# Kernel tuning notes

Hardware: AMD Instinct MI355X
Metric: run time of the kernel (lower is better)

## Reference

```python
import jax, jax.numpy as jnp
import numpy as np

B, C, H, W = 16, 64, 128, 128
HX, HY = 64, 64


def _rnn_scan(x, Wih, Whh, bih, bhh):
    """Vanilla tanh RNN, batch_first. x: [N, T, Cin] -> [N, T, Hh]."""
    # precompute input projection with one big GEMM
    pre = jnp.einsum('ntc,hc->nth', x, Wih) + bih + bhh  # [N,T,Hh]
    N = x.shape[0]
    h0 = jnp.zeros((N, Whh.shape[0]), dtype=x.dtype)

    def step(h, p):
        h = jnp.tanh(p + h @ Whh.T)
        return h, h

    _, ys = jax.lax.scan(step, h0, jnp.swapaxes(pre, 0, 1))  # [T,N,Hh]
    return jnp.swapaxes(ys, 0, 1)


def setup_inputs() -> dict:
    key = jax.random.key(0)
    ks = jax.random.split(key, 9)
    sx = 1.0 / np.sqrt(HX)
    sy = 1.0 / np.sqrt(HY)
    return {
        'x': jax.random.normal(ks[0], (B, C, H, W), dtype=jnp.float32),
        'Wih_x': jax.random.uniform(ks[1], (HX, C), jnp.float32, -sx, sx),
        'Whh_x': jax.random.uniform(ks[2], (HX, HX), jnp.float32, -sx, sx),
        'bih_x': jax.random.uniform(ks[3], (HX,), jnp.float32, -sx, sx),
        'bhh_x': jax.random.uniform(ks[4], (HX,), jnp.float32, -sx, sx),
        'Wih_y': jax.random.uniform(ks[5], (HY, HX), jnp.float32, -sy, sy),
        'Whh_y': jax.random.uniform(ks[6], (HY, HY), jnp.float32, -sy, sy),
        'bih_y': jax.random.uniform(ks[7], (HY,), jnp.float32, -sy, sy),
        'bhh_y': jax.random.uniform(ks[8], (HY,), jnp.float32, -sy, sy),
    }


def reference(x, Wih_x, Whh_x, bih_x, bhh_x, Wih_y, Whh_y, bih_y, bhh_y):
    b, c, h, w = x.shape
    # X-axis RNN: scan along width, sequences are rows
    xw = jnp.transpose(x, (0, 2, 3, 1)).reshape(b * h, w, c)  # [B*H, W, C]
    out_x = _rnn_scan(xw, Wih_x, Whh_x, bih_x, bhh_x)          # [B*H, W, HX]
    # Y-axis RNN: scan along height, sequences are columns
    xy = out_x.reshape(b, h, w, HX)
    xy = jnp.transpose(xy, (0, 2, 1, 3)).reshape(b * w, h, HX)  # [B*W, H, HX]
    out_y = _rnn_scan(xy, Wih_y, Whh_y, bih_y, bhh_y)           # [B*W, H, HY]
    out = out_y.reshape(b, w, h, HY)
    return jnp.transpose(out, (0, 3, 2, 1))  # [B, HY, H, W]
```

## Files before the change

### kernel.cpp

```cpp
#include <hip/hip_runtime.h>
#include <stdint.h>


#define TLEN 128
#define NSEQ 2048
#define PSH (NSEQ*64)
#define GT 16

typedef __bf16   bf16x8 __attribute__((ext_vector_type(8)));
typedef _Float16 f16x8  __attribute__((ext_vector_type(8)));
typedef _Float16 f16x4  __attribute__((ext_vector_type(4)));
typedef float    f32x4  __attribute__((ext_vector_type(4)));
typedef unsigned short u16x4 __attribute__((ext_vector_type(4)));
typedef unsigned short u16x8 __attribute__((ext_vector_type(8)));

static __device__ __forceinline__ unsigned int fbits(float f){
    union { float f; unsigned int u; } v; v.f = f; return v.u;
}
static __device__ __forceinline__ float ubits(unsigned int u){
    union { unsigned int u; float f; } v; v.u = u; return v.f;
}
static __device__ __forceinline__ float bf2f(unsigned short s){ return ubits(((unsigned int)s) << 16); }
static __device__ __forceinline__ unsigned short f2bf(float f){
    unsigned int u = fbits(f);
    return (unsigned short)((u + 0x7FFFu + ((u >> 16) & 1u)) >> 16);
}
static __device__ __forceinline__ __bf16 us2b(unsigned short s){
    union { unsigned short u; __bf16 b; } v; v.u = s; return v.b;
}
static __device__ __forceinline__ unsigned short h2us(_Float16 h){
    union { _Float16 h; unsigned short s; } v; v.h = h; return v.s;
}
struct bfpair { __bf16 hi, lo; };
static __device__ __forceinline__ bfpair splitf(float f){
    unsigned short h = f2bf(f);
    bfpair r; r.hi = us2b(h); r.lo = us2b(f2bf(f - bf2f(h))); return r;
}
static __device__ __forceinline__ float fast_tanh(float x){
    float e = __builtin_amdgcn_exp2f(x * 2.8853900817779268f);
    return 1.0f - 2.0f * __builtin_amdgcn_rcpf(e + 1.0f);
}

__global__ __launch_bounds__(256) void k_proj0(const float* __restrict__ A,
                                               const float* __restrict__ Wih,
                                               const float* __restrict__ b1,
                                               const float* __restrict__ b2,
                                               _Float16* __restrict__ pre){
    __shared__ alignas(16) unsigned short lds_t[2][4][16][64];
    int lane = threadIdx.x & 63;
    int wv   = threadIdx.x >> 6;
    int q    = lane >> 4, l15 = lane & 15;

    bf16x8 Whi[4][2], Wlo[4][2];
#pragma unroll
    for (int n = 0; n < 4; n++)
#pragma unroll
        for (int kc = 0; kc < 2; kc++){
            const float* p = Wih + (n * 16 + l15) * 64 + kc * 32 + q * 8;
#pragma unroll
            for (int i = 0; i < 8; i++){
                bfpair s = splitf(p[i]);
                Whi[n][kc][i] = s.hi; Wlo[n][kc][i] = s.lo;
            }
        }
    float bias[4];
#pragma unroll
    for (int n = 0; n < 4; n++){
        int j = n * 16 + l15;
        bias[n] = b1[j] + b2[j];
    }

    int row0 = blockIdx.x * 128 + wv * 32;

    float av[2][2][8];
#pragma unroll
    for (int mi = 0; mi < 2; mi++){
        int r = row0 + mi * 16 + l15;
        int b = r >> 14, hw = r & 16383;
        const float* xb = A + (size_t)b * 1048576 + hw;
#pragma unroll
        for (int kc = 0; kc < 2; kc++)
#pragma unroll
            for (int i = 0; i < 8; i++)
                av[mi][kc][i] = xb[(size_t)(kc * 32 + q * 8 + i) * 16384];
    }

#pragma unroll
    for (int mi = 0; mi < 2; mi++){
        int rb = row0 + mi * 16;
        bf16x8 Ahi[2], Alo[2];
#pragma unroll
        for (int kc = 0; kc < 2; kc++)
#pragma unroll
            for (int i = 0; i < 8; i++){
                bfpair s = splitf(av[mi][kc][i]);
                Ahi[kc][i] = s.hi; Alo[kc][i] = s.lo;
            }
        f32x4 acc[4];
#pragma unroll
        for (int n = 0; n < 4; n++) acc[n] = (f32x4){bias[n], bias[n], bias[n], bias[n]};
#pragma unroll
        for (int n = 0; n < 4; n++)
#pragma unroll
            for (int kc = 0; kc < 2; kc++){
                acc[n] = __builtin_amdgcn_mfma_f32_16x16x32_bf16(Ahi[kc], Whi[n][kc], acc[n], 0, 0, 0);
                acc[n] = __builtin_amdgcn_mfma_f32_16x16x32_bf16(Alo[kc], Whi[n][kc], acc[n], 0, 0, 0);
                acc[n] = __builtin_amdgcn_mfma_f32_16x16x32_bf16(Ahi[kc], Wlo[n][kc], acc[n], 0, 0, 0);
            }
        int bT = rb >> 14, hT = (rb >> 7) & 127, wBase = rb & 127;
        size_t seqOff = (size_t)bT * 128 + hT;
#pragma unroll
        for (int n = 0; n < 4; n++)
#pragma unroll
            for (int rr = 0; rr < 4; rr++)
                lds_t[mi][wv][q * 4 + rr][n * 16 + l15] = h2us((_Float16)acc[n][rr]);
#pragma unroll
        for (int k = 0; k < 2; k++){
            int wp = (lane >> 3) + k * 8;
            int j8 = (lane & 7) * 8;
            u16x8 v = *(const u16x8*)&lds_t[mi][wv][wp][j8];
            *(u16x8*)(pre + ((size_t)(wBase + wp) * NSEQ + seqOff) * 64 + j8) = v;
        }
    }
}

template<int PASS>
__global__ __launch_bounds__(256) void k_scan(const _Float16* __restrict__ pre,
                                              const float* __restrict__ Whh,
                                              const float* __restrict__ Wy,
                                              const float* __restrict__ by1,
                                              const float* __restrict__ by2,
                                              _Float16* __restrict__ prey,
                                              float* __restrict__ outf){
    __shared__ alignas(16) unsigned short hbuf[2][16][64];
    int lane = threadIdx.x & 63;
    int wv   = threadIdx.x >> 6;
    int q = lane >> 4, l15 = lane & 15;
    int n0 = blockIdx.x * 16;
    int j0 = wv * 16 + q * 4;

    f16x8 Af[2];
#pragma unroll
    for (int kc = 0; kc < 2; kc++){
        const float* p = Whh + (wv * 16 + l15) * 64 + kc * 32 + q * 8;
#pragma unroll
        for (int i = 0; i < 8; i++)
            Af[kc][i] = (_Float16)p[i];
    }
    f16x8 Yf[2];
    f32x4 biasy = (f32x4){0.f, 0.f, 0.f, 0.f};
    if constexpr (PASS == 0){
#pragma unroll
        for (int kc = 0; kc < 2; kc++){
            const float* p = Wy + (wv * 16 + l15) * 64 + kc * 32 + q * 8;
#pragma unroll
            for (int i = 0; i < 8; i++)
                Yf[kc][i] = (_Float16)p[i];
        }
#pragma unroll
        for (int r = 0; r < 4; r++) biasy[r] = by1[j0 + r] + by2[j0 + r];
    }

    f16x8 Bf[2];
#pragma unroll
    for (int kc = 0; kc < 2; kc++)
#pragma unroll
        for (int i = 0; i < 8; i++) Bf[kc][i] = (_Float16)0.f;

    int bb = n0 >> 7, low7 = n0 & 127;

    const _Float16* pb = pre + (size_t)(n0 + l15) * 64 + j0;
    size_t spy = (size_t)(low7 + l15) * NSEQ + (size_t)bb * 128;

    int e   = l15 & 7;
    int wj  = (((j0 >> 3) ^ e) << 3) | (j0 & 7);
    int rj0 = ((q)     ^ e) << 3;
    int rj1 = ((4 + q) ^ e) << 3;

    f16x4 ps[GT];
    u16x4 prey_st[GT];
    f32x4 outst[GT];

    for (int g = 0; g < TLEN / GT; g++){
        int G = g * GT;
#pragma unroll
        for (int u = 0; u < GT; u++)
            ps[u] = *(const f16x4*)(pb + (size_t)(G + u) * PSH);

#pragma unroll
        for (int u = 0; u < GT; u++){
            int t = G + u;
            f32x4 a = (f32x4){(float)ps[u][0], (float)ps[u][1], (float)ps[u][2], (float)ps[u][3]};
            a = __builtin_amdgcn_mfma_f32_16x16x32_f16(Af[0], Bf[0], a, 0, 0, 0);
            a = __builtin_amdgcn_mfma_f32_16x16x32_f16(Af[1], Bf[1], a, 0, 0, 0);
            if constexpr (PASS == 0){
                f32x4 y = biasy;
                y = __builtin_amdgcn_mfma_f32_16x16x32_f16(Yf[0], Bf[0], y, 0, 0, 0);
                y = __builtin_amdgcn_mfma_f32_16x16x32_f16(Yf[1], Bf[1], y, 0, 0, 0);
#pragma unroll
                for (int r = 0; r < 4; r++)
                    prey_st[u][r] = h2us((_Float16)y[r]);
            }

            u16x4 h4;
#pragma unroll
            for (int r = 0; r < 4; r++){
                float tv = fast_tanh(a[r]);
                if constexpr (PASS == 1) outst[u][r] = tv;
                h4[r] = h2us((_Float16)tv);
            }
            int par = t & 1;
            *(u16x4*)&hbuf[par][l15][wj] = h4;
            __syncthreads();
            Bf[0] = *(const f16x8*)&hbuf[par][l15][rj0];
            Bf[1] = *(const f16x8*)&hbuf[par][l15][rj1];
        }
        if constexpr (PASS == 0){
#pragma unroll
            for (int u = 0; u < GT; u++){
                int tp = G - 1 + u;
                if (tp >= 0)
                    *(u16x4*)(prey + (spy + tp) * 64 + j0) = prey_st[u];
            }
        } else {
#pragma unroll
            for (int u = 0; u < GT; u++)
#pragma unroll
                for (int r = 0; r < 4; r++)
                    outf[((size_t)(bb * 64 + j0 + r) * TLEN + (G + u)) * 128 + low7 + l15] = outst[u][r];
        }
    }
    if constexpr (PASS == 0){
        f32x4 y = biasy;
        y = __builtin_amdgcn_mfma_f32_16x16x32_f16(Yf[0], Bf[0], y, 0, 0, 0);
        y = __builtin_amdgcn_mfma_f32_16x16x32_f16(Yf[1], Bf[1], y, 0, 0, 0);
        u16x4 pv;
#pragma unroll
        for (int r = 0; r < 4; r++)
            pv[r] = h2us((_Float16)y[r]);
        *(u16x4*)(prey + (spy + (TLEN - 1)) * 64 + j0) = pv;
    }
}

extern "C" void kernel_launch(void* const* d_in, const int* in_sizes, int n_in,
                              void* d_out, int out_size, void* d_ws, size_t ws_size,
                              hipStream_t stream){
    (void)in_sizes; (void)n_in; (void)out_size; (void)ws_size;
    const float* x    = (const float*)d_in[0];
    const float* Wihx = (const float*)d_in[1];
    const float* Whhx = (const float*)d_in[2];
    const float* bihx = (const float*)d_in[3];
    const float* bhhx = (const float*)d_in[4];
    const float* Wihy = (const float*)d_in[5];
    const float* Whhy = (const float*)d_in[6];
    const float* bihy = (const float*)d_in[7];
    const float* bhhy = (const float*)d_in[8];
    _Float16* prex = (_Float16*)d_ws;
    _Float16* prey = prex + (size_t)NSEQ * TLEN * 64;
    float* of = (float*)d_out;

    k_proj0 <<<2048, 256, 0, stream>>>(x, Wihx, bihx, bhhx, prex);
    k_scan<0><<<128, 256, 0, stream>>>(prex, Whhx, Wihy, bihy, bhhy, prey, nullptr);
    k_scan<1><<<128, 256, 0, stream>>>(prey, Whhy, nullptr, nullptr, nullptr, nullptr, of);
}
```

Baseline: 227.8 us.

## Double-buffer scan input slabs and hand-code LDS exchange with inline asm

```diff
diff --git a/kernel.cpp b/kernel.cpp
--- a/kernel.cpp
+++ b/kernel.cpp
@@ -123,6 +123,72 @@
         }
     }
 }
+
+
+#define PARS 2048u
+
+#define LOADSLAB(PS, GB)                                       \
+    _Pragma("unroll")                                          \
+    for (int u_ = 0; u_ < GT; u_++)                            \
+        PS[u_] = *(const f16x4*)(pb + (size_t)((GB) + u_) * PSH);
+
+#define TICKS(PS, GB)                                                           \
+    _Pragma("unroll")                                                           \
+    for (int u = 0; u < GT; u++){                                               \
+        int t = (GB) + u;                                                       \
+        f32x4 a = (f32x4){(float)PS[u][0], (float)PS[u][1],                     \
+                          (float)PS[u][2], (float)PS[u][3]};                    \
+        a = __builtin_amdgcn_mfma_f32_16x16x32_f16(Af[0], Bf[0], a, 0, 0, 0);   \
+        a = __builtin_amdgcn_mfma_f32_16x16x32_f16(Af[1], Bf[1], a, 0, 0, 0);   \
+        if constexpr (PASS == 0){                                               \
+            f32x4 y = biasy;                                                    \
+            y = __builtin_amdgcn_mfma_f32_16x16x32_f16(Yf[0], Bf[0], y, 0, 0, 0); \
+            y = __builtin_amdgcn_mfma_f32_16x16x32_f16(Yf[1], Bf[1], y, 0, 0, 0); \
+            _Pragma("unroll")                                                   \
+            for (int r = 0; r < 4; r++)                                         \
+                prey_st[u][r] = h2us((_Float16)y[r]);                           \
+        }                                                                       \
+        u16x4 h4;                                                               \
+        _Pragma("unroll")                                                       \
+        for (int r = 0; r < 4; r++){                                            \
+            float tv = fast_tanh(a[r]);                                         \
+            if constexpr (PASS == 1) outst[u][r] = tv;                          \
+            h4[r] = h2us((_Float16)tv);                                         \
+        }                                                                       \
+        unsigned int pofs = (unsigned int)((t & 1) ? PARS : 0u);                \
+        unsigned int wa = wj_off + pofs;                                        \
+        asm volatile("ds_write_b64 %0, %1\n\t"                                  \
+                     "s_waitcnt lgkmcnt(0)\n\t"                                 \
+                     "s_barrier"                                                \
+                     :: "v"(wa), "v"(h4) : "memory");                           \
+        unsigned int ra0 = rj0_off + pofs;                                      \
+        unsigned int ra1 = rj1_off + pofs;                                      \
+        f16x8 nb0, nb1;                                                         \
+        asm volatile("ds_read_b128 %0, %2\n\t"                                  \
+                     "ds_read_b128 %1, %3\n\t"                                  \
+                     "s_waitcnt lgkmcnt(0)"                                     \
+                     : "=&v"(nb0), "=&v"(nb1)                                   \
+                     : "v"(ra0), "v"(ra1) : "memory");                          \
+        __builtin_amdgcn_sched_barrier(0);                                      \
+        Bf[0] = nb0; Bf[1] = nb1;                                               \
+    }
+
+#define GSTORE(GB)                                                              \
+    if constexpr (PASS == 0){                                                   \
+        _Pragma("unroll")                                                       \
+        for (int u = 0; u < GT; u++){                                           \
+            int tp = (GB) - 1 + u;                                              \
+            if (tp >= 0)                                                        \
+                *(u16x4*)(prey + (spy + tp) * 64 + j0) = prey_st[u];            \
+        }                                                                       \
+    } else {                                                                    \
+        _Pragma("unroll")                                                       \
+        for (int u = 0; u < GT; u++)                                            \
+            _Pragma("unroll")                                                   \
+            for (int r = 0; r < 4; r++)                                         \
+                outf[((size_t)(bb * 64 + j0 + r) * TLEN + ((GB) + u)) * 128     \
+                     + low7 + l15] = outst[u][r];                               \
+    }
 
 template<int PASS>
 __global__ __launch_bounds__(256) void k_scan(const _Float16* __restrict__ pre,
@@ -177,58 +243,23 @@
     int rj0 = ((q)     ^ e) << 3;
     int rj1 = ((4 + q) ^ e) << 3;
 
-    f16x4 ps[GT];
+    unsigned int wj_off  = (unsigned int)(uintptr_t)&hbuf[0][l15][wj];
+    unsigned int rj0_off = (unsigned int)(uintptr_t)&hbuf[0][l15][rj0];
+    unsigned int rj1_off = (unsigned int)(uintptr_t)&hbuf[0][l15][rj1];
+
+    f16x4 psA[GT], psB[GT];
     u16x4 prey_st[GT];
     f32x4 outst[GT];
 
-    for (int g = 0; g < TLEN / GT; g++){
-        int G = g * GT;
-#pragma unroll
-        for (int u = 0; u < GT; u++)
-            ps[u] = *(const f16x4*)(pb + (size_t)(G + u) * PSH);
-
-#pragma unroll
-        for (int u = 0; u < GT; u++){
-            int t = G + u;
-            f32x4 a = (f32x4){(float)ps[u][0], (float)ps[u][1], (float)ps[u][2], (float)ps[u][3]};
-            a = __builtin_amdgcn_mfma_f32_16x16x32_f16(Af[0], Bf[0], a, 0, 0, 0);
-            a = __builtin_amdgcn_mfma_f32_16x16x32_f16(Af[1], Bf[1], a, 0, 0, 0);
-            if constexpr (PASS == 0){
-                f32x4 y = biasy;
-                y = __builtin_amdgcn_mfma_f32_16x16x32_f16(Yf[0], Bf[0], y, 0, 0, 0);
-                y = __builtin_amdgcn_mfma_f32_16x16x32_f16(Yf[1], Bf[1], y, 0, 0, 0);
-#pragma unroll
-                for (int r = 0; r < 4; r++)
-                    prey_st[u][r] = h2us((_Float16)y[r]);
-            }
-
-            u16x4 h4;
-#pragma unroll
-            for (int r = 0; r < 4; r++){
-                float tv = fast_tanh(a[r]);
-                if constexpr (PASS == 1) outst[u][r] = tv;
-                h4[r] = h2us((_Float16)tv);
-            }
-            int par = t & 1;
-            *(u16x4*)&hbuf[par][l15][wj] = h4;
-            __syncthreads();
-            Bf[0] = *(const f16x8*)&hbuf[par][l15][rj0];
-            Bf[1] = *(const f16x8*)&hbuf[par][l15][rj1];
-        }
-        if constexpr (PASS == 0){
-#pragma unroll
-            for (int u = 0; u < GT; u++){
-                int tp = G - 1 + u;
-                if (tp >= 0)
-                    *(u16x4*)(prey + (spy + tp) * 64 + j0) = prey_st[u];
-            }
-        } else {
-#pragma unroll
-            for (int u = 0; u < GT; u++)
-#pragma unroll
-                for (int r = 0; r < 4; r++)
-                    outf[((size_t)(bb * 64 + j0 + r) * TLEN + (G + u)) * 128 + low7 + l15] = outst[u][r];
-        }
+    LOADSLAB(psA, 0);
+    for (int gp = 0; gp < 4; gp++){
+        int G0 = gp * 32;
+        LOADSLAB(psB, G0 + 16);
+        TICKS(psA, G0);
+        GSTORE(G0);
+        if (gp < 3) LOADSLAB(psA, G0 + 32);
+        TICKS(psB, G0 + 16);
+        GSTORE(G0 + 16);
     }
     if constexpr (PASS == 0){
         f32x4 y = biasy;
```

New measurement: 228.9 us. About the same (+0.5%).
